# Kernel tuning notes

Hardware: AMD Instinct MI355X
Metric: run time of the kernel (lower is better)

## Reference

```python
import jax, jax.numpy as jnp
import numpy as np

B = 2048        # graphs
MAX_LEN = 254   # nodes per graph (pad target)
DIM = 64
NF = 78         # num_features_xd
DEG = 8
N = B * MAX_LEN         # 520192 nodes
E = N * DEG             # 4161536 edges
BN_EPS = 1e-5
LN_EPS = 1e-5


def setup_inputs() -> dict:
    key = jax.random.key(0)
    ks = jax.random.split(key, 24)
    x = jax.random.normal(ks[0], (N, NF), jnp.float32)
    # intra-graph random edges: (src, dst) within the same graph
    g = jax.random.randint(ks[1], (E,), 0, B)
    src = g * MAX_LEN + jax.random.randint(ks[2], (E,), 0, MAX_LEN)
    dst = g * MAX_LEN + jax.random.randint(ks[3], (E,), 0, MAX_LEN)
    edge_index = jnp.stack([src, dst]).astype(jnp.int32)
    batch = (jnp.arange(N) // MAX_LEN).astype(jnp.int32)
    batch_len = jnp.full((B,), MAX_LEN, jnp.int32)

    def lin(k, fan_in, shape):
        return jax.random.uniform(k, shape, jnp.float32, -1.0, 1.0) / np.sqrt(fan_in)

    # conv1 MLP: 78->64->64
    w1a = lin(ks[4], NF, (NF, DIM)); b1a = lin(ks[5], NF, (DIM,))
    w1b = lin(ks[6], DIM, (DIM, DIM)); b1b = lin(ks[7], DIM, (DIM,))
    # convs 2-5 stacked: 64->64->64
    Wa = lin(ks[8], DIM, (4, DIM, DIM)); ba = lin(ks[9], DIM, (4, DIM))
    Wb = lin(ks[10], DIM, (4, DIM, DIM)); bb = lin(ks[11], DIM, (4, DIM))
    bn_gamma = jnp.ones((5, DIM), jnp.float32)
    bn_beta = jnp.zeros((5, DIM), jnp.float32)
    fc_w = lin(ks[12], DIM, (DIM, DIM)); fc_b = lin(ks[13], DIM, (DIM,))
    ln_gamma = jnp.ones((DIM,), jnp.float32)
    ln_beta = jnp.zeros((DIM,), jnp.float32)
    return {
        "x": x, "edge_index": edge_index, "batch": batch,
        "batch_len": batch_len, "max_len": MAX_LEN,
        "w1a": w1a, "b1a": b1a, "w1b": w1b, "b1b": b1b,
        "Wa": Wa, "ba": ba, "Wb": Wb, "bb": bb,
        "bn_gamma": bn_gamma, "bn_beta": bn_beta,
        "fc_w": fc_w, "fc_b": fc_b,
        "ln_gamma": ln_gamma, "ln_beta": ln_beta,
    }


def _gin_layer(h, src, dst, n, W1, b1, W2, b2, gamma, beta):
    # GINConv (eps=0): z_i = MLP(x_i + sum_{j->i} x_j), then ReLU, then BatchNorm (batch stats)
    agg = jax.ops.segment_sum(h[src], dst, num_segments=n)
    z = h + agg
    z = jnp.maximum(z @ W1 + b1, 0.0) @ W2 + b2
    z = jnp.maximum(z, 0.0)
    mean = z.mean(axis=0)
    var = jnp.square(z - mean).mean(axis=0)  # biased var, as torch BN training
    return (z - mean) * jax.lax.rsqrt(var + BN_EPS) * gamma + beta


def reference(x, edge_index, batch, batch_len, max_len,
              w1a, b1a, w1b, b1b, Wa, ba, Wb, bb,
              bn_gamma, bn_beta, fc_w, fc_b, ln_gamma, ln_beta):
    n = x.shape[0]
    src, dst = edge_index[0], edge_index[1]
    h = _gin_layer(x, src, dst, n, w1a, b1a, w1b, b1b, bn_gamma[0], bn_beta[0])
    for i in range(4):
        h = _gin_layer(h, src, dst, n, Wa[i], ba[i], Wb[i], bb[i],
                       bn_gamma[i + 1], bn_beta[i + 1])
    # get_nodes_att_f: pad per-graph node features to [B, max_len, dim]
    nb = batch_len.shape[0]
    offsets = jnp.cumsum(batch_len) - batch_len            # start index of each graph
    pos = jnp.arange(n, dtype=jnp.int32) - offsets[batch]  # node position within graph
    x_seq = jnp.zeros((nb, max_len, h.shape[1]), h.dtype).at[batch, pos].set(h)
    # global_add_pool + fc + relu + (dropout eval: identity) + layernorm
    pooled = jax.ops.segment_sum(h, batch, num_segments=nb)
    y = jnp.maximum(pooled @ fc_w + fc_b, 0.0)
    mu = y.mean(axis=-1, keepdims=True)
    var = jnp.square(y - mu).mean(axis=-1, keepdims=True)
    y = (y - mu) * jax.lax.rsqrt(var + LN_EPS) * ln_gamma + ln_beta
    return (x_seq, y)
```

## Files before the change

kernel.cpp:

```cpp
#include <hip/hip_runtime.h>

#define NGRAPH 2048
#define MAXLEN 254
#define NNODE 520192
#define NEDGE 4161536
#define NF 78
#define BN_EPS 1e-5f
#define LN_EPS 1e-5f

__global__ __launch_bounds__(256) void k_init(int* __restrict__ deg, float* __restrict__ stats,
                                              int* __restrict__ total) {
    int i = blockIdx.x * 256 + threadIdx.x;
    deg[i] = 0;
    if (blockIdx.x == 0) {
        for (int j = threadIdx.x; j < 5 * 128; j += 256) stats[j] = 0.f;
        if (threadIdx.x == 0) *total = 0;
    }
}

__global__ __launch_bounds__(256) void k_hist(const int* __restrict__ ei, int* __restrict__ deg) {
    int e = blockIdx.x * 256 + threadIdx.x;
    atomicAdd(&deg[ei[NEDGE + e]], 1);
}

__global__ __launch_bounds__(256) void k_scan(const int* __restrict__ deg,
                                              int* __restrict__ row_start,
                                              int* __restrict__ cursor, int* __restrict__ total) {
    int i = blockIdx.x * 256 + threadIdx.x;
    int d = deg[i];
    int lane = threadIdx.x & 63;
    int v = d;
#pragma unroll
    for (int o = 1; o < 64; o <<= 1) {
        int t = __shfl_up(v, o, 64);
        if (lane >= o) v += t;
    }
    int wsum = __shfl(v, 63, 64);
    int base = 0;
    if (lane == 63) base = atomicAdd(total, wsum);
    base = __shfl(base, 63, 64);
    int start = base + v - d;
    row_start[i] = start;
    cursor[i] = start;
}

__global__ __launch_bounds__(256) void k_fill(const int* __restrict__ ei, int* __restrict__ cursor,
                                              unsigned char* __restrict__ elist) {
    int e = blockIdx.x * 256 + threadIdx.x;
    int s = ei[e];
    int d = ei[NEDGE + e];
    int g = d / MAXLEN;
    int p = atomicAdd(&cursor[d], 1);
    elist[p] = (unsigned char)(s - g * MAXLEN);
}

template <int FOLD>
__global__ __launch_bounds__(256) void k_gather(const float* __restrict__ h,
                                                const unsigned char* __restrict__ elist,
                                                const int* __restrict__ row_start,
                                                const int* __restrict__ deg,
                                                const float* __restrict__ stats,
                                                const float* __restrict__ gamma,
                                                const float* __restrict__ beta,
                                                float* __restrict__ acc) {
    size_t t = (size_t)blockIdx.x * 256 + threadIdx.x;
    int node = (int)(t >> 4);
    int g4 = (int)(t & 15) * 4;
    int rs = row_start[node];
    int dg = deg[node];
    int base = (node / MAXLEN) * MAXLEN;
    const float4 h0 = *(const float4*)(h + ((size_t)node << 6) + g4);
    float a0 = h0.x, a1 = h0.y, a2 = h0.z, a3 = h0.w;
    for (int e = 0; e < dg; e++) {
        int s = base + elist[rs + e];
        float4 v = *(const float4*)(h + ((size_t)s << 6) + g4);
        a0 += v.x; a1 += v.y; a2 += v.z; a3 += v.w;
    }
    if (FOLD) {
        const float invN = 1.0f / NNODE;
        float k = (float)(1 + dg);
        float r[4] = {a0, a1, a2, a3};
#pragma unroll
        for (int j = 0; j < 4; j++) {
            float mean = stats[g4 + j] * invN;
            float var = stats[64 + g4 + j] * invN - mean * mean;
            float sc = gamma[g4 + j] * rsqrtf(var + BN_EPS);
            float bi = beta[g4 + j] - mean * sc;
            r[j] = r[j] * sc + k * bi;
        }
        a0 = r[0]; a1 = r[1]; a2 = r[2]; a3 = r[3];
    }
    *(float4*)(acc + ((size_t)node << 6) + g4) = make_float4(a0, a1, a2, a3);
}

__global__ __launch_bounds__(256) void k_gemm78(const float* __restrict__ x,
                                                const float* __restrict__ W,
                                                float* __restrict__ out) {
    __shared__ float sW[NF * 64];
    for (int i = threadIdx.x; i < NF * 64; i += 256) sW[i] = W[i];
    __syncthreads();
    int node = blockIdx.x * 256 + threadIdx.x;
    const float* xr = x + (size_t)node * NF;
    float a[64];
#pragma unroll
    for (int c = 0; c < 64; c++) a[c] = 0.f;
    for (int k2 = 0; k2 < NF / 2; k2++) {
        float2 xv = ((const float2*)xr)[k2];
        const float* w0 = sW + (2 * k2) * 64;
#pragma unroll
        for (int c = 0; c < 64; c++) a[c] += xv.x * w0[c];
#pragma unroll
        for (int c = 0; c < 64; c++) a[c] += xv.y * w0[64 + c];
    }
    float* orow = out + ((size_t)node << 6);
#pragma unroll
    for (int c = 0; c < 64; c += 4)
        *(float4*)(orow + c) = make_float4(a[c], a[c + 1], a[c + 2], a[c + 3]);
}

__device__ __forceinline__ void second_matmul(const float (&a)[64], const float* __restrict__ sW2,
                                              const float* __restrict__ sb2,
                                              float* __restrict__ orow) {
#pragma unroll
    for (int cb = 0; cb < 64; cb += 16) {
        float o[16];
#pragma unroll
        for (int j = 0; j < 16; j++) o[j] = sb2[cb + j];
#pragma unroll
        for (int k = 0; k < 64; k++) {
            float ak = a[k];
#pragma unroll
            for (int j = 0; j < 16; j++) o[j] += ak * sW2[k * 64 + cb + j];
        }
#pragma unroll
        for (int j = 0; j < 16; j += 4)
            *(float4*)(orow + cb + j) =
                make_float4(fmaxf(o[j], 0.f), fmaxf(o[j + 1], 0.f),
                            fmaxf(o[j + 2], 0.f), fmaxf(o[j + 3], 0.f));
    }
}

__global__ __launch_bounds__(256) void k_mlp_tail(const float* __restrict__ zin,
                                                  const float* __restrict__ b1,
                                                  const float* __restrict__ W2,
                                                  const float* __restrict__ b2,
                                                  float* __restrict__ out) {
    __shared__ float sW2[64 * 64];
    __shared__ float sb1[64], sb2[64];
    for (int i = threadIdx.x; i < 64 * 64; i += 256) sW2[i] = W2[i];
    if (threadIdx.x < 64) { sb1[threadIdx.x] = b1[threadIdx.x]; sb2[threadIdx.x] = b2[threadIdx.x]; }
    __syncthreads();
    int node = blockIdx.x * 256 + threadIdx.x;
    const float* zr = zin + ((size_t)node << 6);
    float a[64];
#pragma unroll
    for (int c = 0; c < 64; c += 4) {
        float4 v = *(const float4*)(zr + c);
        a[c]     = fmaxf(v.x + sb1[c], 0.f);
        a[c + 1] = fmaxf(v.y + sb1[c + 1], 0.f);
        a[c + 2] = fmaxf(v.z + sb1[c + 2], 0.f);
        a[c + 3] = fmaxf(v.w + sb1[c + 3], 0.f);
    }
    second_matmul(a, sW2, sb2, out + ((size_t)node << 6));
}

__global__ __launch_bounds__(256) void k_mlp_dual(const float* __restrict__ zin,
                                                  const float* __restrict__ W1,
                                                  const float* __restrict__ b1,
                                                  const float* __restrict__ W2,
                                                  const float* __restrict__ b2,
                                                  float* __restrict__ out) {
    __shared__ float sW1[64 * 64];
    __shared__ float sW2[64 * 64];
    __shared__ float sb1[64], sb2[64];
    for (int i = threadIdx.x; i < 64 * 64; i += 256) { sW1[i] = W1[i]; sW2[i] = W2[i]; }
    if (threadIdx.x < 64) { sb1[threadIdx.x] = b1[threadIdx.x]; sb2[threadIdx.x] = b2[threadIdx.x]; }
    __syncthreads();
    int node = blockIdx.x * 256 + threadIdx.x;
    const float* zr = zin + ((size_t)node << 6);
    float a[64];
#pragma unroll
    for (int c = 0; c < 64; c++) a[c] = sb1[c];
    for (int k4 = 0; k4 < 16; k4++) {
        float4 xv = ((const float4*)zr)[k4];
        const float* w = sW1 + k4 * 256;
#pragma unroll
        for (int c = 0; c < 64; c++) a[c] += xv.x * w[c];
#pragma unroll
        for (int c = 0; c < 64; c++) a[c] += xv.y * w[64 + c];
#pragma unroll
        for (int c = 0; c < 64; c++) a[c] += xv.z * w[128 + c];
#pragma unroll
        for (int c = 0; c < 64; c++) a[c] += xv.w * w[192 + c];
    }
#pragma unroll
    for (int c = 0; c < 64; c++) a[c] = fmaxf(a[c], 0.f);
    second_matmul(a, sW2, sb2, out + ((size_t)node << 6));
}

__global__ __launch_bounds__(256) void k_bnstats(const float* __restrict__ h,
                                                 float* __restrict__ stats) {
    __shared__ float ss[128];
    if (threadIdx.x < 128) ss[threadIdx.x] = 0.f;
    __syncthreads();
    int tid = blockIdx.x * 256 + threadIdx.x;
    int c4 = (tid & 15) * 4;
    float s0 = 0, s1 = 0, s2 = 0, s3 = 0, q0 = 0, q1 = 0, q2 = 0, q3 = 0;
    const float4* p = (const float4*)h;
    for (size_t i = tid; i < (size_t)NNODE * 16; i += 65536) {
        float4 v = p[i];
        s0 += v.x; q0 += v.x * v.x;
        s1 += v.y; q1 += v.y * v.y;
        s2 += v.z; q2 += v.z * v.z;
        s3 += v.w; q3 += v.w * v.w;
    }
    atomicAdd(&ss[c4], s0);      atomicAdd(&ss[c4 + 1], s1);
    atomicAdd(&ss[c4 + 2], s2);  atomicAdd(&ss[c4 + 3], s3);
    atomicAdd(&ss[64 + c4], q0); atomicAdd(&ss[64 + c4 + 1], q1);
    atomicAdd(&ss[64 + c4 + 2], q2); atomicAdd(&ss[64 + c4 + 3], q3);
    __syncthreads();
    if (threadIdx.x < 128) atomicAdd(&stats[threadIdx.x], ss[threadIdx.x]);
}

__global__ __launch_bounds__(256) void k_bnapply(float* __restrict__ h,
                                                 const float* __restrict__ stats,
                                                 const float* __restrict__ gamma,
                                                 const float* __restrict__ beta) {
    size_t i = (size_t)blockIdx.x * 256 + threadIdx.x;
    int c0 = (int)(i & 15) * 4;
    const float invN = 1.0f / NNODE;
    float4 v = ((const float4*)h)[i];
    float sc[4], bi[4];
#pragma unroll
    for (int j = 0; j < 4; j++) {
        float mean = stats[c0 + j] * invN;
        float var = stats[64 + c0 + j] * invN - mean * mean;
        float s = gamma[c0 + j] * rsqrtf(var + BN_EPS);
        sc[j] = s;
        bi[j] = beta[c0 + j] - mean * s;
    }
    v.x = v.x * sc[0] + bi[0];
    v.y = v.y * sc[1] + bi[1];
    v.z = v.z * sc[2] + bi[2];
    v.w = v.w * sc[3] + bi[3];
    ((float4*)h)[i] = v;
}

__global__ __launch_bounds__(256) void k_final(const float* __restrict__ h,
                                               const float* __restrict__ fcw,
                                               const float* __restrict__ fcb,
                                               const float* __restrict__ lng,
                                               const float* __restrict__ lnb,
                                               float* __restrict__ y) {
    int b = blockIdx.x;
    int q = threadIdx.x >> 6;
    int c = threadIdx.x & 63;
    const float* base = h + (size_t)b * MAXLEN * 64;
    float s = 0.f;
    for (int p = q; p < MAXLEN; p += 4) s += base[p * 64 + c];
    __shared__ float sp[4][64];
    sp[q][c] = s;
    __syncthreads();
    __shared__ float pooled[64];
    if (threadIdx.x < 64) pooled[c] = sp[0][c] + sp[1][c] + sp[2][c] + sp[3][c];
    __syncthreads();
    if (threadIdx.x < 64) {
        float accv = fcb[c];
        for (int k = 0; k < 64; k++) accv += pooled[k] * fcw[k * 64 + c];
        accv = fmaxf(accv, 0.f);
        float t = accv;
        for (int o = 32; o; o >>= 1) t += __shfl_xor(t, o, 64);
        float mu = t * (1.0f / 64.0f);
        float d = accv - mu;
        float t2 = d * d;
        for (int o = 32; o; o >>= 1) t2 += __shfl_xor(t2, o, 64);
        float var = t2 * (1.0f / 64.0f);
        y[(size_t)b * 64 + c] = d * rsqrtf(var + LN_EPS) * lng[c] + lnb[c];
    }
}

extern "C" void kernel_launch(void* const* d_in, const int* in_sizes, int n_in,
                              void* d_out, int out_size, void* d_ws, size_t ws_size,
                              hipStream_t stream) {
    const float* x   = (const float*)d_in[0];
    const int*   ei  = (const int*)d_in[1];
    const float* w1a = (const float*)d_in[5];
    const float* b1a = (const float*)d_in[6];
    const float* w1b = (const float*)d_in[7];
    const float* b1b = (const float*)d_in[8];
    const float* Wa  = (const float*)d_in[9];
    const float* ba  = (const float*)d_in[10];
    const float* Wb  = (const float*)d_in[11];
    const float* bb  = (const float*)d_in[12];
    const float* bng = (const float*)d_in[13];
    const float* bnb = (const float*)d_in[14];
    const float* fcw = (const float*)d_in[15];
    const float* fcb = (const float*)d_in[16];
    const float* lng = (const float*)d_in[17];
    const float* lnb = (const float*)d_in[18];

    float* h   = (float*)d_out;
    float* y   = h + (size_t)NNODE * 64;
    float* acc = (float*)d_ws;
    float* stats = acc + (size_t)NNODE * 64;
    int* deg       = (int*)(stats + 5 * 128);
    int* row_start = deg + NNODE;
    int* cursor    = row_start + NNODE;
    int* total     = cursor + NNODE;
    unsigned char* elist = (unsigned char*)(total + 4);

    const int NB_NODE = NNODE / 256;
    const int NB_VEC  = NNODE * 16 / 256;
    const int NB_EDGE = NEDGE / 256;
    (void)in_sizes; (void)n_in; (void)out_size; (void)ws_size;

    k_init<<<NB_NODE, 256, 0, stream>>>(deg, stats, total);
    k_hist<<<NB_EDGE, 256, 0, stream>>>(ei, deg);
    k_scan<<<NB_NODE, 256, 0, stream>>>(deg, row_start, cursor, total);
    k_fill<<<NB_EDGE, 256, 0, stream>>>(ei, cursor, elist);

    k_gemm78<<<NB_NODE, 256, 0, stream>>>(x, w1a, h);
    k_gather<0><<<NB_VEC, 256, 0, stream>>>(h, elist, row_start, deg, nullptr, nullptr, nullptr, acc);
    k_mlp_tail<<<NB_NODE, 256, 0, stream>>>(acc, b1a, w1b, b1b, h);
    k_bnstats<<<256, 256, 0, stream>>>(h, stats);

    for (int L = 1; L <= 4; L++) {
        k_gather<1><<<NB_VEC, 256, 0, stream>>>(h, elist, row_start, deg,
                                                stats + (L - 1) * 128,
                                                bng + (size_t)(L - 1) * 64,
                                                bnb + (size_t)(L - 1) * 64, acc);
        k_mlp_dual<<<NB_NODE, 256, 0, stream>>>(acc, Wa + (size_t)(L - 1) * 4096,
                                                ba + (size_t)(L - 1) * 64,
                                                Wb + (size_t)(L - 1) * 4096,
                                                bb + (size_t)(L - 1) * 64, h);
        k_bnstats<<<256, 256, 0, stream>>>(h, stats + L * 128);
    }

    k_bnapply<<<NB_VEC, 256, 0, stream>>>(h, stats + 4 * 128, bng + 4 * 64, bnb + 4 * 64);
    k_final<<<NGRAPH, 256, 0, stream>>>(h, fcw, fcb, lng, lnb, y);
}
```

Baseline: 2.803 ms.

## Replace CSR edge build with fixed-capacity ELL lists and XCD-swizzled gather

Replaces the histogram, scan and fill CSR construction with one build kernel. It writes each incoming neighbour byte into a fixed 32-slot per-node row, indexed by an atomic degree counter. The gather reads the neighbour bytes four at a time as packed 32-bit words. It also remaps block indices in chunks of eight so neighbouring graph nodes tend to land on the same XCD and share L2. The cost is padded edge storage and an unchecked assumption that no node has more than 32 incoming edges.

```diff
diff --git a/kernel.cpp b/kernel.cpp
--- a/kernel.cpp
+++ b/kernel.cpp
@@ -5,76 +5,58 @@
 #define NNODE 520192
 #define NEDGE 4161536
 #define NF 78
+#define CAP 32
 #define BN_EPS 1e-5f
 #define LN_EPS 1e-5f
 
-__global__ __launch_bounds__(256) void k_init(int* __restrict__ deg, float* __restrict__ stats,
-                                              int* __restrict__ total) {
+__global__ __launch_bounds__(256) void k_init(int* __restrict__ deg, float* __restrict__ stats) {
     int i = blockIdx.x * 256 + threadIdx.x;
     deg[i] = 0;
     if (blockIdx.x == 0) {
         for (int j = threadIdx.x; j < 5 * 128; j += 256) stats[j] = 0.f;
-        if (threadIdx.x == 0) *total = 0;
-    }
-}
-
-__global__ __launch_bounds__(256) void k_hist(const int* __restrict__ ei, int* __restrict__ deg) {
-    int e = blockIdx.x * 256 + threadIdx.x;
-    atomicAdd(&deg[ei[NEDGE + e]], 1);
-}
-
-__global__ __launch_bounds__(256) void k_scan(const int* __restrict__ deg,
-                                              int* __restrict__ row_start,
-                                              int* __restrict__ cursor, int* __restrict__ total) {
-    int i = blockIdx.x * 256 + threadIdx.x;
-    int d = deg[i];
-    int lane = threadIdx.x & 63;
-    int v = d;
-#pragma unroll
-    for (int o = 1; o < 64; o <<= 1) {
-        int t = __shfl_up(v, o, 64);
-        if (lane >= o) v += t;
-    }
-    int wsum = __shfl(v, 63, 64);
-    int base = 0;
-    if (lane == 63) base = atomicAdd(total, wsum);
-    base = __shfl(base, 63, 64);
-    int start = base + v - d;
-    row_start[i] = start;
-    cursor[i] = start;
-}
-
-__global__ __launch_bounds__(256) void k_fill(const int* __restrict__ ei, int* __restrict__ cursor,
-                                              unsigned char* __restrict__ elist) {
+    }
+}
+
+__global__ __launch_bounds__(256) void k_build(const int* __restrict__ ei,
+                                               int* __restrict__ deg,
+                                               unsigned char* __restrict__ elist) {
     int e = blockIdx.x * 256 + threadIdx.x;
     int s = ei[e];
     int d = ei[NEDGE + e];
     int g = d / MAXLEN;
-    int p = atomicAdd(&cursor[d], 1);
-    elist[p] = (unsigned char)(s - g * MAXLEN);
+    int r = atomicAdd(&deg[d], 1);
+    elist[(size_t)d * CAP + r] = (unsigned char)(s - g * MAXLEN);
 }
 
 template <int FOLD>
 __global__ __launch_bounds__(256) void k_gather(const float* __restrict__ h,
                                                 const unsigned char* __restrict__ elist,
-                                                const int* __restrict__ row_start,
                                                 const int* __restrict__ deg,
                                                 const float* __restrict__ stats,
                                                 const float* __restrict__ gamma,
                                                 const float* __restrict__ beta,
                                                 float* __restrict__ acc) {
-    size_t t = (size_t)blockIdx.x * 256 + threadIdx.x;
+    const int CHUNK = (NNODE * 16 / 256) / 8;
+    int lb = (int)(blockIdx.x & 7) * CHUNK + (int)(blockIdx.x >> 3);
+    size_t t = (size_t)lb * 256 + threadIdx.x;
     int node = (int)(t >> 4);
     int g4 = (int)(t & 15) * 4;
-    int rs = row_start[node];
     int dg = deg[node];
     int base = (node / MAXLEN) * MAXLEN;
     const float4 h0 = *(const float4*)(h + ((size_t)node << 6) + g4);
     float a0 = h0.x, a1 = h0.y, a2 = h0.z, a3 = h0.w;
-    for (int e = 0; e < dg; e++) {
-        int s = base + elist[rs + e];
-        float4 v = *(const float4*)(h + ((size_t)s << 6) + g4);
-        a0 += v.x; a1 += v.y; a2 += v.z; a3 += v.w;
+    const unsigned* row = (const unsigned*)(elist + (size_t)node * CAP);
+    int ne4 = (dg + 3) >> 2;
+    for (int e4 = 0; e4 < ne4; e4++) {
+        unsigned pk = row[e4];
+#pragma unroll
+        for (int j = 0; j < 4; j++) {
+            if (4 * e4 + j < dg) {
+                int s = base + (int)((pk >> (8 * j)) & 255u);
+                float4 v = *(const float4*)(h + ((size_t)s << 6) + g4);
+                a0 += v.x; a1 += v.y; a2 += v.z; a3 += v.w;
+            }
+        }
     }
     if (FOLD) {
         const float invN = 1.0f / NNODE;
@@ -303,29 +285,24 @@
     float* y   = h + (size_t)NNODE * 64;
     float* acc = (float*)d_ws;
     float* stats = acc + (size_t)NNODE * 64;
-    int* deg       = (int*)(stats + 5 * 128);
-    int* row_start = deg + NNODE;
-    int* cursor    = row_start + NNODE;
-    int* total     = cursor + NNODE;
-    unsigned char* elist = (unsigned char*)(total + 4);
+    int* deg = (int*)(stats + 5 * 128);
+    unsigned char* elist = (unsigned char*)(deg + NNODE);
 
     const int NB_NODE = NNODE / 256;
     const int NB_VEC  = NNODE * 16 / 256;
     const int NB_EDGE = NEDGE / 256;
     (void)in_sizes; (void)n_in; (void)out_size; (void)ws_size;
 
-    k_init<<<NB_NODE, 256, 0, stream>>>(deg, stats, total);
-    k_hist<<<NB_EDGE, 256, 0, stream>>>(ei, deg);
-    k_scan<<<NB_NODE, 256, 0, stream>>>(deg, row_start, cursor, total);
-    k_fill<<<NB_EDGE, 256, 0, stream>>>(ei, cursor, elist);
+    k_init<<<NB_NODE, 256, 0, stream>>>(deg, stats);
+    k_build<<<NB_EDGE, 256, 0, stream>>>(ei, deg, elist);
 
     k_gemm78<<<NB_NODE, 256, 0, stream>>>(x, w1a, h);
-    k_gather<0><<<NB_VEC, 256, 0, stream>>>(h, elist, row_start, deg, nullptr, nullptr, nullptr, acc);
+    k_gather<0><<<NB_VEC, 256, 0, stream>>>(h, elist, deg, nullptr, nullptr, nullptr, acc);
     k_mlp_tail<<<NB_NODE, 256, 0, stream>>>(acc, b1a, w1b, b1b, h);
     k_bnstats<<<256, 256, 0, stream>>>(h, stats);
 
     for (int L = 1; L <= 4; L++) {
-        k_gather<1><<<NB_VEC, 256, 0, stream>>>(h, elist, row_start, deg,
+        k_gather<1><<<NB_VEC, 256, 0, stream>>>(h, elist, deg,
                                                 stats + (L - 1) * 128,
                                                 bng + (size_t)(L - 1) * 64,
                                                 bnb + (size_t)(L - 1) * 64, acc);
```

Result: faster. 2.321 ms (-17.2%).
